# Kernel optimization log

Measured on AMD Instinct MI355X. Metric: run time of the kernel, lower is better.

## Reference

```python
import jax, jax.numpy as jnp
import numpy as np

G = 4      # groups (conv groups == offset groups)
KS = 3     # kernel size
DIL = 1    # dilation
PAD = 1    # padding = dilation
EPS = 1e-5 # InstanceNorm eps


def setup_inputs() -> dict:
    key = jax.random.key(0)
    k1, k2, k3, k4, k5 = jax.random.split(key, 5)
    B, C, D, H, W = 4, 64, 8, 64, 64
    Cout = 64
    Cg = C // G
    x = jax.random.normal(k1, (B, C, D, H, W), jnp.float32)
    # small offset-conv weights so predicted offsets stay within a few pixels
    w_off = jax.random.normal(k2, (2 * KS * KS * G, Cg, KS, KS), jnp.float32) * 0.01
    b_off = jax.random.normal(k3, (2 * KS * KS * G,), jnp.float32) * 0.01
    w_dc = jax.random.normal(k4, (Cout, Cg, KS, KS), jnp.float32) * (1.0 / np.sqrt(Cg * KS * KS))
    b_dc = jax.random.normal(k5, (Cout,), jnp.float32) * 0.01
    return {"x": x, "w_off": w_off, "b_off": b_off, "w_dc": w_dc, "b_dc": b_dc}


def reference(x, w_off, b_off, w_dc, b_dc):
    B, C, D, H, W = x.shape
    N = B * D
    K = KS * KS
    Cg = C // G
    # torch .view(B*D, C, H, W) is a row-major reshape of the flat buffer
    x2 = x.reshape(N, C, H, W)

    # grouped 3x3 offset conv, same padding
    off = jax.lax.conv_general_dilated(
        x2, w_off, (1, 1), [(PAD, PAD), (PAD, PAD)],
        rhs_dilation=(DIL, DIL), feature_group_count=G,
        dimension_numbers=("NCHW", "OIHW", "NCHW"),
    ) + b_off[None, :, None, None]
    off = off.reshape(N, G, K, 2, H, W)        # (y, x) offset per group/kernel-pt
    dy, dx = off[:, :, :, 0], off[:, :, :, 1]  # [N,G,K,H,W]

    # base sampling grid per kernel point
    ki, kj = jnp.meshgrid(jnp.arange(KS), jnp.arange(KS), indexing="ij")
    ki = ki.reshape(K); kj = kj.reshape(K)
    base_y = (jnp.arange(H)[None, :] - PAD + ki[:, None] * DIL).astype(jnp.float32)  # [K,H]
    base_x = (jnp.arange(W)[None, :] - PAD + kj[:, None] * DIL).astype(jnp.float32)  # [K,W]
    py = base_y[None, None, :, :, None] + dy   # [N,G,K,H,W]
    px = base_x[None, None, :, None, :] + dx

    y0 = jnp.floor(py); x0 = jnp.floor(px)
    ly = py - y0; lx = px - x0
    y0i = y0.astype(jnp.int32); x0i = x0.astype(jnp.int32)

    xg = x2.reshape(N, G, Cg, H * W)
    gather = jax.vmap(jax.vmap(lambda xf, idx: xf[:, idx]))  # over N, G

    def corner(yi, xi, w):
        valid = (yi >= 0) & (yi < H) & (xi >= 0) & (xi < W)   # zero-pad OOB
        idx = jnp.clip(yi, 0, H - 1) * W + jnp.clip(xi, 0, W - 1)
        v = gather(xg, idx.reshape(N, G, -1)).reshape(N, G, Cg, K, H, W)
        return v * (w * valid)[:, :, None]                    # broadcast over Cg

    val = (corner(y0i,     x0i,     (1 - ly) * (1 - lx))
         + corner(y0i,     x0i + 1, (1 - ly) * lx)
         + corner(y0i + 1, x0i,     ly * (1 - lx))
         + corner(y0i + 1, x0i + 1, ly * lx))                 # [N,G,Cg,K,H,W]

    wg = w_dc.reshape(G, -1, Cg, K)                           # [G,Coutg,Cg,K]
    out = jnp.einsum("gock,ngckhw->ngohw", wg, val).reshape(N, -1, H, W)
    out = out + b_dc[None, :, None, None]

    # InstanceNorm2d (affine=False, biased var) + exact GELU
    m = out.mean((-2, -1), keepdims=True)
    v = out.var((-2, -1), keepdims=True)
    out = jax.nn.gelu((out - m) * jax.lax.rsqrt(v + EPS), approximate=False)

    Cout = out.shape[1]
    return out.reshape(B, D, Cout, H, W).transpose(0, 2, 1, 3, 4)  # [B,Cout,D,H,W]
```

## Files before the change

kernel.cpp:

```cpp
#include <hip/hip_runtime.h>
#include <hip/hip_bf16.h>
#include <math.h>

#define HW 4096
#define NN 32
#define W68 68
#define SLICE (68 * 68)

typedef __attribute__((ext_vector_type(8))) short bf16x8;
typedef __attribute__((ext_vector_type(4))) float f32x4;

__device__ inline unsigned short bfbits(float a) {
    __hip_bfloat16 h = __float2bfloat16(a);
    unsigned short u;
    __builtin_memcpy(&u, &h, 2);
    return u;
}
__device__ inline unsigned packbf(float a, float b) {
    return (unsigned)bfbits(a) | ((unsigned)bfbits(b) << 16);
}
__device__ inline float bflo(unsigned u) { return __uint_as_float(u << 16); }
__device__ inline float bfhi(unsigned u) { return __uint_as_float(u & 0xffff0000u); }

__device__ inline void bilin8(uint4 A, uint4 B, uint4 C, uint4 D,
                              const float* ww, float* val) {
    const unsigned* ua = (const unsigned*)&A;
    const unsigned* ub = (const unsigned*)&B;
    const unsigned* uc = (const unsigned*)&C;
    const unsigned* ud = (const unsigned*)&D;
    #pragma unroll
    for (int j = 0; j < 4; j++) {
        val[2*j]   = ww[0]*bflo(ua[j]) + ww[1]*bflo(ub[j]) + ww[2]*bflo(uc[j]) + ww[3]*bflo(ud[j]);
        val[2*j+1] = ww[0]*bfhi(ua[j]) + ww[1]*bfhi(ub[j]) + ww[2]*bfhi(uc[j]) + ww[3]*bfhi(ud[j]);
    }
}

__global__ __launch_bounds__(256) void transpose_x(const float* __restrict__ x,
                                                   unsigned short* __restrict__ xT,
                                                   const float* __restrict__ w_off,
                                                   const float* __restrict__ w_dc,
                                                   unsigned short* __restrict__ wperm)
{
    int bx = blockIdx.x;
    int t = threadIdx.x;

    if (bx < 120) {
        int idx = bx * 256 + t;
        int g = idx / 7680;
        int r3 = idx - g * 7680;
        int which = r3 / 2560;
        int r = r3 - which * 2560;
        int j = r & 7;
        int rest = r >> 3;
        int nn_ = rest & 15; rest >>= 4;
        int q_ = rest & 3, kp_ = rest >> 2;
        int k = q_ * 8 + j;
        int c = k & 15, tt = kp_ * 2 + (k >> 4);
        float v = 0.f;
        if (tt < 9) {
            if (which == 0)      v = w_dc[(g * 16 + nn_) * 144 + c * 9 + tt];
            else if (which == 1) v = w_off[(g * 18 + nn_) * 144 + c * 9 + tt];
            else if (nn_ < 2)    v = w_off[(g * 18 + 16 + nn_) * 144 + c * 9 + tt];
        }
        wperm[idx] = bfbits(v);
    }

    __shared__ float tile[256 * 17];
    int n = bx >> 6, g = (bx >> 4) & 3, chunk = bx & 15;
    const float* xb = x + (size_t)(n * 64 + g * 16) * HW + chunk * 256;

    #pragma unroll
    for (int r = 0; r < 16; r++) {
        int idx = r * 256 + t;
        int c = idx >> 8, p = idx & 255;
        tile[p * 17 + c] = xb[c * HW + p];
    }
    __syncthreads();

    unsigned short* ob = xT + (size_t)(n * 4 + g) * SLICE * 16;
    #pragma unroll
    for (int r = 0; r < 2; r++) {
        int idx = r * 256 + t;
        int p = idx >> 1, half = idx & 1;
        int pos = chunk * 256 + p;
        int h = pos >> 6, w = pos & 63;
        const float* tp = &tile[p * 17 + half * 8];
        uint4 v;
        v.x = packbf(tp[0], tp[1]);
        v.y = packbf(tp[2], tp[3]);
        v.z = packbf(tp[4], tp[5]);
        v.w = packbf(tp[6], tp[7]);
        *(uint4*)(ob + ((size_t)((h + 2) * W68 + (w + 2)) * 16 + half * 8)) = v;
    }
}

__global__ __launch_bounds__(256, 4) void fused_conv(const unsigned short* __restrict__ xT,
                                                     const unsigned short* __restrict__ wperm,
                                                     const float* __restrict__ b_off,
                                                     const float* __restrict__ b_dc,
                                                     float* __restrict__ outpre)
{
    __shared__ __attribute__((aligned(8))) unsigned short off_lds[256 * 20];

    int bx = blockIdx.x;
    int n = bx >> 6, g = (bx >> 4) & 3, chunk = bx & 15;
    int t = threadIdx.x;
    int lane = t & 63, wv = t >> 6;
    int nn = lane & 15, q = lane >> 4;
    int t2 = q >> 1, chh = q & 1;

    const unsigned short* wpg = wperm + g * 7680;
    const unsigned short* xw = xT + (size_t)(n * 4 + g) * SLICE * 16 + chh * 8;

    int pls[4]; float fy[4], fx[4]; int basep[4];
    #pragma unroll
    for (int s = 0; s < 4; s++) {
        int pl = (wv * 4 + s) * 16 + nn;
        int pos = chunk * 256 + pl;
        int h = pos >> 6, w = pos & 63;
        pls[s] = pl;
        fy[s] = (float)(h - 1);
        fx[s] = (float)(w - 1);
        basep[s] = (h + 1) * W68 + (w + 1);
    }

    {
        bf16x8 pb0[5], pb1[5];
        #pragma unroll
        for (int kp = 0; kp < 5; kp++) {
            int fo = ((kp * 4 + q) * 16 + nn) * 8;
            pb0[kp] = *(const bf16x8*)(wpg + 2560 + fo);
            pb1[kp] = *(const bf16x8*)(wpg + 5120 + fo);
        }

        f32x4 acc0[4], acc1[4];
        float bv0 = b_off[g * 18 + nn];
        float bv1 = (nn < 2) ? b_off[g * 18 + 16 + nn] : 0.f;
        #pragma unroll
        for (int s = 0; s < 4; s++)
            #pragma unroll
            for (int r = 0; r < 4; r++) { acc0[s][r] = bv0; acc1[s][r] = bv1; }

        uint4 xv[2][4];
        auto stage1 = [&](int kp) {
            int ki = t2 ? (2 * kp + 1) / 3 : (2 * kp) / 3;
            int kj = t2 ? (2 * kp + 1) % 3 : (2 * kp) % 3;
            int xo = ki * W68 + kj;
            int sl = kp & 1;
            #pragma unroll
            for (int s = 0; s < 4; s++)
                xv[sl][s] = *(const uint4*)(xw + (size_t)(basep[s] + xo) * 16);
        };
        stage1(0);
        #pragma unroll
        for (int kp = 0; kp < 5; kp++) {
            if (kp < 4) stage1(kp + 1);
            int sl = kp & 1;
            #pragma unroll
            for (int s = 0; s < 4; s++) {
                bf16x8 af = *(bf16x8*)&xv[sl][s];
                acc0[s] = __builtin_amdgcn_mfma_f32_16x16x32_bf16(af, pb0[kp], acc0[s], 0, 0, 0);
                acc1[s] = __builtin_amdgcn_mfma_f32_16x16x32_bf16(af, pb1[kp], acc1[s], 0, 0, 0);
            }
        }

        #pragma unroll
        for (int s = 0; s < 4; s++) {
            int pl = (wv * 4 + s) * 16 + q * 4;
            #pragma unroll
            for (int r = 0; r < 4; r++) {
                off_lds[(pl + r) * 20 + nn] = bfbits(acc0[s][r]);
                if (nn < 2)
                    off_lds[(pl + r) * 20 + 16 + nn] = bfbits(acc1[s][r]);
            }
        }
        off_lds[t * 20 + 18] = 0;
        off_lds[t * 20 + 19] = 0;
    }

    bf16x8 bwr[5];
    #pragma unroll
    for (int kp = 0; kp < 5; kp++)
        bwr[kp] = *(const bf16x8*)(wpg + ((kp * 4 + q) * 16 + nn) * 8);

    __syncthreads();

    f32x4 acc[4];
    float bv = b_dc[g * 16 + nn];
    #pragma unroll
    for (int s = 0; s < 4; s++)
        #pragma unroll
        for (int r = 0; r < 4; r++) acc[s][r] = bv;

    uint4 RA[2], RB[2], RC[2], RD[2];
    float rw[2][4];

    auto stage = [&](int u) {
        int kp = u >> 2, s = u & 3, sl = u & 1;
        int ki = t2 ? (2 * kp + 1) / 3 : (2 * kp) / 3;
        int kj = t2 ? (2 * kp + 1) % 3 : (2 * kp) % 3;
        int tap2 = 4 * kp + 2 * t2;
        unsigned uo = *(const unsigned*)&off_lds[pls[s] * 20 + tap2];
        float py = fy[s] + (float)ki + bflo(uo);
        float px = fx[s] + (float)kj + bfhi(uo);
        float y0f = fminf(fmaxf(floorf(py), -2.f), 64.f);
        float x0f = fminf(fmaxf(floorf(px), -2.f), 64.f);
        float ly = py - y0f, lx = px - x0f;
        float my = 1.f - ly, mx = 1.f - lx;
        rw[sl][0] = my * mx; rw[sl][1] = my * lx;
        rw[sl][2] = ly * mx; rw[sl][3] = ly * lx;
        int base = (int)(y0f * 68.f + x0f) + 138;
        const unsigned short* p0 = xw + (size_t)base * 16;
        RA[sl] = *(const uint4*)(p0);
        RB[sl] = *(const uint4*)(p0 + 16);
        RC[sl] = *(const uint4*)(p0 + W68 * 16);
        RD[sl] = *(const uint4*)(p0 + W68 * 16 + 16);
    };
    auto consume = [&](int u) {
        int kp = u >> 2, s = u & 3, sl = u & 1;
        float val[8];
        bilin8(RA[sl], RB[sl], RC[sl], RD[sl], rw[sl], val);
        bf16x8 af;
        #pragma unroll
        for (int j = 0; j < 8; j++) af[j] = (short)bfbits(val[j]);
        acc[s] = __builtin_amdgcn_mfma_f32_16x16x32_bf16(af, bwr[kp], acc[s], 0, 0, 0);
    };

    stage(0);
    #pragma unroll
    for (int u = 0; u < 20; u++) {
        if (u < 19) stage(u + 1);
        consume(u);
    }

    float* op = outpre + (size_t)(n * 64 + g * 16) * HW;
    #pragma unroll
    for (int s = 0; s < 4; s++) {
        int pbase = chunk * 256 + (wv * 4 + s) * 16 + q * 4;
        #pragma unroll
        for (int r = 0; r < 4; r++)
            op[nn * HW + pbase + r] = acc[s][r];
    }
}

__global__ __launch_bounds__(256) void norm_gelu(const float* __restrict__ outpre,
                                                 float* __restrict__ out)
{
    __shared__ float red[8];
    int bx = blockIdx.x;
    int n  = bx >> 6;
    int co = bx & 63;
    int t  = threadIdx.x;

    const float4* base = (const float4*)(outpre + (size_t)(n * 64 + co) * HW);
    float4 v[4];
    float s = 0.f, sq = 0.f;
    #pragma unroll
    for (int r = 0; r < 4; r++) {
        v[r] = base[t + r * 256];
        s  += v[r].x + v[r].y + v[r].z + v[r].w;
        sq  = fmaf(v[r].x, v[r].x, sq);
        sq  = fmaf(v[r].y, v[r].y, sq);
        sq  = fmaf(v[r].z, v[r].z, sq);
        sq  = fmaf(v[r].w, v[r].w, sq);
    }
    #pragma unroll
    for (int o2 = 32; o2 > 0; o2 >>= 1) {
        s  += __shfl_down(s,  o2, 64);
        sq += __shfl_down(sq, o2, 64);
    }
    int wid = t >> 6, lane = t & 63;
    if (lane == 0) { red[wid] = s; red[4 + wid] = sq; }
    __syncthreads();
    float S  = red[0] + red[1] + red[2] + red[3];
    float SQ = red[4] + red[5] + red[6] + red[7];
    float mean = S * (1.f / 4096.f);
    float var  = SQ * (1.f / 4096.f) - mean * mean;
    float rstd = rsqrtf(var + 1e-5f);

    int b = n >> 3, d = n & 7;
    float4* outp = (float4*)(out + ((size_t)(b * 64 + co) * 8 + d) * HW);
    #pragma unroll
    for (int r = 0; r < 4; r++) {
        float xs[4] = {v[r].x, v[r].y, v[r].z, v[r].w};
        float4 res;
        float* rp = (float*)&res;
        #pragma unroll
        for (int qq = 0; qq < 4; qq++) {
            float xn = (xs[qq] - mean) * rstd;
            float u = xn * (1.5957691f + 0.0713548162f * xn * xn);
            float e = __expf(-u);
            rp[qq] = xn * __frcp_rn(1.f + e);
        }
        outp[t + r * 256] = res;
    }
}

extern "C" void kernel_launch(void* const* d_in, const int* in_sizes, int n_in,
                              void* d_out, int out_size, void* d_ws, size_t ws_size,
                              hipStream_t stream) {
    const float* x     = (const float*)d_in[0];
    const float* w_off = (const float*)d_in[1];
    const float* b_off = (const float*)d_in[2];  (void)b_off;
    const float* w_dc  = (const float*)d_in[3];
    const float* b_dc  = (const float*)d_in[4];
    float* out = (float*)d_out;

    unsigned short* wperm = (unsigned short*)d_ws;
    unsigned short* xTb   = wperm + 30720;
    float* outpre = (float*)(xTb + (size_t)NN * 4 * SLICE * 16);

    hipMemsetAsync(d_ws, 0, 61440 + (size_t)NN * 4 * SLICE * 16 * 2, stream);

    transpose_x<<<2048, 256, 0, stream>>>(x, xTb, w_off, w_dc, wperm);
    fused_conv <<<2048, 256, 0, stream>>>(xTb, wperm,
                                          (const float*)d_in[2], b_dc, outpre);
    norm_gelu  <<<2048, 256, 0, stream>>>(outpre, out);
}
```

Measured before the change: 145.7 us.

## Stage swizzled input row window in LDS and drop workspace memset

Each block copies a 9-row by 68-column window of the padded bf16 input into shared memory, using an XOR swizzle. Both the offset convolution and the deformable bilinear gather then read that window instead of global memory. Gathers whose sampled row falls outside the window fall back to the old global loads, chosen per lane after a wave-wide check. The full-workspace memset is removed because transpose_x now writes zeros to the padding border itself, and the weight register loads are hoisted before the first barrier. This trades more LDS use, which may lower occupancy, and an extra divergent branch for less global and L2 gather traffic and one fewer large memory fill.

```diff
diff --git a/kernel.cpp b/kernel.cpp
--- a/kernel.cpp
+++ b/kernel.cpp
@@ -21,6 +21,10 @@
 }
 __device__ inline float bflo(unsigned u) { return __uint_as_float(u << 16); }
 __device__ inline float bfhi(unsigned u) { return __uint_as_float(u & 0xffff0000u); }
+
+__device__ inline int xsw(int x, int c8) {
+    return ((x << 5) | (c8 << 4)) ^ (((x >> 2) & 1) << 4);
+}
 
 __device__ inline void bilin8(uint4 A, uint4 B, uint4 C, uint4 D,
                               const float* ww, float* val) {
@@ -92,6 +96,18 @@
         v.w = packbf(tp[6], tp[7]);
         *(uint4*)(ob + ((size_t)((h + 2) * W68 + (w + 2)) * 16 + half * 8)) = v;
     }
+
+    if (t < 66) {
+        int j = t >> 1, half = t & 1;
+        int hp = chunk * 33 + j;
+        int R, C;
+        if (hp < 136)      { R = hp / 68;               C = hp % 68; }
+        else if (hp < 272) { int q2 = hp - 136; R = 66 + q2 / 68; C = q2 % 68; }
+        else               { int q2 = hp - 272; R = 2 + (q2 >> 2);
+                             C = (q2 & 3); C = C < 2 ? C : C + 64; }
+        uint4 z = {0, 0, 0, 0};
+        *(uint4*)(ob + ((size_t)(R * W68 + C) * 16 + half * 8)) = z;
+    }
 }
 
 __global__ __launch_bounds__(256, 4) void fused_conv(const unsigned short* __restrict__ xT,
@@ -100,7 +116,8 @@
                                                      const float* __restrict__ b_dc,
                                                      float* __restrict__ outpre)
 {
-    __shared__ __attribute__((aligned(8))) unsigned short off_lds[256 * 20];
+    __shared__ __attribute__((aligned(16))) unsigned short xwin[9 * 1088];
+    __shared__ __attribute__((aligned(8)))  unsigned short off_lds[256 * 20];
 
     int bx = blockIdx.x;
     int n = bx >> 6, g = (bx >> 4) & 3, chunk = bx & 15;
@@ -108,11 +125,35 @@
     int lane = t & 63, wv = t >> 6;
     int nn = lane & 15, q = lane >> 4;
     int t2 = q >> 1, chh = q & 1;
+    int R0 = chunk * 4;
 
     const unsigned short* wpg = wperm + g * 7680;
-    const unsigned short* xw = xT + (size_t)(n * 4 + g) * SLICE * 16 + chh * 8;
-
-    int pls[4]; float fy[4], fx[4]; int basep[4];
+    const unsigned short* xsl = xT + (size_t)(n * 4 + g) * SLICE * 16;
+    const unsigned short* xw  = xsl + chh * 8;
+
+    {
+        uint4 sv[5]; int sof[5];
+        #pragma unroll
+        for (int k = 0; k < 5; k++) {
+            int sidx = k * 256 + t;
+            int row = sidx / 136;
+            int rem = sidx - row * 136;
+            int xx = rem >> 1, c8 = rem & 1;
+            int Rg = R0 + row; Rg = Rg > 67 ? 67 : Rg;
+            bool ok = sidx < 1224;
+            uint4 z = {0, 0, 0, 0};
+            sv[k] = ok ? *(const uint4*)(xsl + ((size_t)(Rg * 68 + xx) * 16 + c8 * 8)) : z;
+            sof[k] = row * 2176 + xsw(xx, c8);
+        }
+        #pragma unroll
+        for (int k = 0; k < 5; k++) {
+            int sidx = k * 256 + t;
+            if (sidx < 1224)
+                *(uint4*)((char*)xwin + sof[k]) = sv[k];
+        }
+    }
+
+    int pls[4]; float fy[4], fx[4]; int rws[4], xbs[4];
     #pragma unroll
     for (int s = 0; s < 4; s++) {
         int pl = (wv * 4 + s) * 16 + nn;
@@ -121,18 +162,22 @@
         pls[s] = pl;
         fy[s] = (float)(h - 1);
         fx[s] = (float)(w - 1);
-        basep[s] = (h + 1) * W68 + (w + 1);
-    }
+        rws[s] = ((wv * 4 + s) >> 2) + 1;
+        xbs[s] = ((wv * 4 + s) & 3) * 16 + nn + 1;
+    }
+
+    bf16x8 pb0[5], pb1[5], bwr[5];
+    #pragma unroll
+    for (int kp = 0; kp < 5; kp++) {
+        int fo = ((kp * 4 + q) * 16 + nn) * 8;
+        pb0[kp] = *(const bf16x8*)(wpg + 2560 + fo);
+        pb1[kp] = *(const bf16x8*)(wpg + 5120 + fo);
+        bwr[kp] = *(const bf16x8*)(wpg + fo);
+    }
+
+    __syncthreads();
 
     {
-        bf16x8 pb0[5], pb1[5];
-        #pragma unroll
-        for (int kp = 0; kp < 5; kp++) {
-            int fo = ((kp * 4 + q) * 16 + nn) * 8;
-            pb0[kp] = *(const bf16x8*)(wpg + 2560 + fo);
-            pb1[kp] = *(const bf16x8*)(wpg + 5120 + fo);
-        }
-
         f32x4 acc0[4], acc1[4];
         float bv0 = b_off[g * 18 + nn];
         float bv1 = (nn < 2) ? b_off[g * 18 + 16 + nn] : 0.f;
@@ -145,11 +190,12 @@
         auto stage1 = [&](int kp) {
             int ki = t2 ? (2 * kp + 1) / 3 : (2 * kp) / 3;
             int kj = t2 ? (2 * kp + 1) % 3 : (2 * kp) % 3;
-            int xo = ki * W68 + kj;
             int sl = kp & 1;
             #pragma unroll
-            for (int s = 0; s < 4; s++)
-                xv[sl][s] = *(const uint4*)(xw + (size_t)(basep[s] + xo) * 16);
+            for (int s = 0; s < 4; s++) {
+                int adr = (rws[s] + ki) * 2176 + xsw(xbs[s] + kj, chh);
+                xv[sl][s] = *(const uint4*)((const char*)xwin + adr);
+            }
         };
         stage1(0);
         #pragma unroll
@@ -177,12 +223,6 @@
         off_lds[t * 20 + 18] = 0;
         off_lds[t * 20 + 19] = 0;
     }
-
-    bf16x8 bwr[5];
-    #pragma unroll
-    for (int kp = 0; kp < 5; kp++)
-        bwr[kp] = *(const bf16x8*)(wpg + ((kp * 4 + q) * 16 + nn) * 8);
-
     __syncthreads();
 
     f32x4 acc[4];
@@ -193,33 +233,49 @@
         for (int r = 0; r < 4; r++) acc[s][r] = bv;
 
     uint4 RA[2], RB[2], RC[2], RD[2];
-    float rw[2][4];
+    float rw_[2][4];
+    int rinw[2], rgb[2];
 
     auto stage = [&](int u) {
         int kp = u >> 2, s = u & 3, sl = u & 1;
         int ki = t2 ? (2 * kp + 1) / 3 : (2 * kp) / 3;
         int kj = t2 ? (2 * kp + 1) % 3 : (2 * kp) % 3;
-        int tap2 = 4 * kp + 2 * t2;
-        unsigned uo = *(const unsigned*)&off_lds[pls[s] * 20 + tap2];
+        unsigned uo = *(const unsigned*)&off_lds[pls[s] * 20 + 4 * kp + 2 * t2];
         float py = fy[s] + (float)ki + bflo(uo);
         float px = fx[s] + (float)kj + bfhi(uo);
         float y0f = fminf(fmaxf(floorf(py), -2.f), 64.f);
         float x0f = fminf(fmaxf(floorf(px), -2.f), 64.f);
         float ly = py - y0f, lx = px - x0f;
         float my = 1.f - ly, mx = 1.f - lx;
-        rw[sl][0] = my * mx; rw[sl][1] = my * lx;
-        rw[sl][2] = ly * mx; rw[sl][3] = ly * lx;
-        int base = (int)(y0f * 68.f + x0f) + 138;
-        const unsigned short* p0 = xw + (size_t)base * 16;
-        RA[sl] = *(const uint4*)(p0);
-        RB[sl] = *(const uint4*)(p0 + 16);
-        RC[sl] = *(const uint4*)(p0 + W68 * 16);
-        RD[sl] = *(const uint4*)(p0 + W68 * 16 + 16);
+        rw_[sl][0] = my * mx; rw_[sl][1] = my * lx;
+        rw_[sl][2] = ly * mx; rw_[sl][3] = ly * lx;
+        int y0 = (int)y0f, x0 = (int)x0f;
+        int lr = y0 + 2 - R0;
+        int inw = ((unsigned)lr <= 7u);
+        int lrc = inw ? lr : 0;
+        int xx = x0 + 2;
+        int a0 = lrc * 2176 + xsw(xx, chh);
+        int a1 = lrc * 2176 + xsw(xx + 1, chh);
+        RA[sl] = *(const uint4*)((const char*)xwin + a0);
+        RB[sl] = *(const uint4*)((const char*)xwin + a1);
+        RC[sl] = *(const uint4*)((const char*)xwin + a0 + 2176);
+        RD[sl] = *(const uint4*)((const char*)xwin + a1 + 2176);
+        rinw[sl] = inw;
+        rgb[sl] = (y0 + 2) * W68 + xx;
     };
     auto consume = [&](int u) {
         int kp = u >> 2, s = u & 3, sl = u & 1;
+        if (!__all(rinw[sl])) {
+            if (!rinw[sl]) {
+                const unsigned short* p0 = xw + (size_t)rgb[sl] * 16;
+                RA[sl] = *(const uint4*)(p0);
+                RB[sl] = *(const uint4*)(p0 + 16);
+                RC[sl] = *(const uint4*)(p0 + W68 * 16);
+                RD[sl] = *(const uint4*)(p0 + W68 * 16 + 16);
+            }
+        }
         float val[8];
-        bilin8(RA[sl], RB[sl], RC[sl], RD[sl], rw[sl], val);
+        bilin8(RA[sl], RB[sl], RC[sl], RD[sl], rw_[sl], val);
         bf16x8 af;
         #pragma unroll
         for (int j = 0; j < 8; j++) af[j] = (short)bfbits(val[j]);
@@ -310,7 +366,6 @@
     unsigned short* xTb   = wperm + 30720;
     float* outpre = (float*)(xTb + (size_t)NN * 4 * SLICE * 16);
 
-    hipMemsetAsync(d_ws, 0, 61440 + (size_t)NN * 4 * SLICE * 16 * 2, stream);
 
     transpose_x<<<2048, 256, 0, stream>>>(x, xTb, w_off, w_dc, wperm);
     fused_conv <<<2048, 256, 0, stream>>>(xTb, wperm,
```

New measurement: 146.8 us. About the same (+0.7%).
